# Performance work log

Hardware: AMD Instinct MI355X
Metric: run time of the kernel (lower is better)

The kernel has to match this reference:

```python
import jax, jax.numpy as jnp
import numpy as np

LN_EPS = 1e-5


def _segment_mean(vals, idx, num_segments):
    s = jax.ops.segment_sum(vals, idx, num_segments=num_segments)
    cnt = jax.ops.segment_sum(jnp.ones((vals.shape[0],), vals.dtype), idx, num_segments=num_segments)
    return s / jnp.maximum(cnt, 1.0)[:, None]


def _sage_layer(x, src, dst, W_l, b_l, W_r, gamma, beta):
    # PyG SAGEConv (mean aggr): out = lin_l(mean_{j in N(i)} x_j) + lin_r(x_i)
    N = x.shape[0]
    agg = _segment_mean(x[src], dst, N)                     # [N, in]
    h = agg @ W_l.T + b_l + x @ W_r.T                       # [N, out]
    mu = jnp.mean(h, axis=-1, keepdims=True)
    var = jnp.mean((h - mu) ** 2, axis=-1, keepdims=True)
    h = (h - mu) * jax.lax.rsqrt(var + LN_EPS) * gamma + beta
    return jax.nn.relu(h)                                   # dropout: eval mode (identity)


def setup_inputs() -> dict:
    key = jax.random.key(0)
    ks = jax.random.split(key, 20)
    N, E, IN, H, OUT, G, C = 50000, 600000, 128, 128, 64, 64, 2

    def glorot(k, fo, fi):
        lim = np.sqrt(6.0 / (fo + fi)).astype(np.float32)
        return jax.random.uniform(k, (fo, fi), jnp.float32, -lim, lim)

    inp = {
        'x': jax.random.normal(ks[0], (N, IN), jnp.float32),
        'edge_index': jax.random.randint(ks[1], (2, E), 0, N, jnp.int64),
        'batch': jnp.sort(jax.random.randint(ks[2], (N,), 0, G, jnp.int64)),
    }
    dims = [(IN, H), (H, H), (H, OUT)]
    for i, (fi, fo) in enumerate(dims):
        inp[f'Wl{i}'] = glorot(ks[3 + 4 * i], fo, fi)
        inp[f'bl{i}'] = jnp.zeros((fo,), jnp.float32)
        inp[f'Wr{i}'] = glorot(ks[4 + 4 * i], fo, fi)
        inp[f'g{i}'] = jnp.ones((fo,), jnp.float32)
        inp[f'be{i}'] = jnp.zeros((fo,), jnp.float32)
    inp['cW1'] = glorot(ks[16], H, 2 * OUT)
    inp['cb1'] = jnp.zeros((H,), jnp.float32)
    inp['cW2'] = glorot(ks[17], C, H)
    inp['cb2'] = jnp.zeros((C,), jnp.float32)
    return inp


def reference(x, edge_index, batch,
              Wl0, bl0, Wr0, g0, be0,
              Wl1, bl1, Wr1, g1, be1,
              Wl2, bl2, Wr2, g2, be2,
              cW1, cb1, cW2, cb2):
    src, dst = edge_index[0], edge_index[1]
    h = _sage_layer(x, src, dst, Wl0, bl0, Wr0, g0, be0)
    h = _sage_layer(h, src, dst, Wl1, bl1, Wr1, g1, be1)
    h = _sage_layer(h, src, dst, Wl2, bl2, Wr2, g2, be2)
    G = 64  # number of graphs
    x_mean = _segment_mean(h, batch, G)                     # [G, out]
    x_max = jax.ops.segment_max(h, batch, num_segments=G)   # [G, out]
    z = jnp.concatenate([x_mean, x_max], axis=-1)           # [G, 2*out]
    z = jax.nn.relu(z @ cW1.T + cb1)
    return z @ cW2.T + cb2                                  # [G, num_classes]
```

## Files before the change

### kernel.cpp

```cpp
#include <hip/hip_runtime.h>

typedef unsigned short ushort_t;
typedef short s16x8 __attribute__((ext_vector_type(8)));
typedef float f32x4 __attribute__((ext_vector_type(4)));

#define LN_EPS 1e-5f

__device__ __forceinline__ float b2f(ushort_t u) {
    return __uint_as_float(((unsigned)u) << 16);
}
__device__ __forceinline__ ushort_t f2b(float f) {
    unsigned b = __float_as_uint(f);
    b += 0x7FFFu + ((b >> 16) & 1u);
    return (ushort_t)(b >> 16);
}
__device__ __forceinline__ unsigned f2b2(float lo, float hi) {
    return (unsigned)f2b(lo) | ((unsigned)f2b(hi) << 16);
}
__device__ __forceinline__ float ldf(const void* p, size_t i, int isF) {
    return isF ? ((const float*)p)[i] : b2f(((const ushort_t*)p)[i]);
}

__global__ void GraphSAGE_36026185678961_kernel() {}

__global__ void k_detect_zero(const void* w0, const void* ei, int* __restrict__ flags,
                              int* __restrict__ deg, float* __restrict__ Z, int N) {
    int i = blockIdx.x * blockDim.x + threadIdx.x;
    if (i < N) deg[i] = 0;
    if (i < 64 * 128) Z[i] = 0.f;
    if (blockIdx.x == 0 && threadIdx.x < 64) {
        int t = threadIdx.x;
        const ushort_t* u = (const ushort_t*)w0;
        int pass = 0;
        #pragma unroll
        for (int k = 0; k < 4; ++k) {
            ushort_t v = u[t * 4 + k];
            int ex = (v >> 7) & 0xFF;
            if (ex == 0 || (ex >= 0x60 && ex <= 0x7E)) pass++;
        }
        const unsigned* w = (const unsigned*)ei;
        int nz = (w[2 * t + 1] != 0u) ? 1 : 0;
        #pragma unroll
        for (int off = 32; off; off >>= 1) {
            pass += __shfl_down(pass, off, 64);
            nz += __shfl_down(nz, off, 64);
        }
        if (t == 0) {
            flags[0] = (pass < 205) ? 1 : 0;
            flags[1] = (nz == 0) ? 1 : 0;
        }
    }
}

__global__ void k_xconv(const void* X, const int* __restrict__ flags,
                        ushort_t* __restrict__ XB, int total4) {
    int idx = blockIdx.x * blockDim.x + threadIdx.x;
    if (idx >= total4) return;
    if (flags[0]) {
        float4 v = ((const float4*)X)[idx];
        ushort4 o;
        o.x = f2b(v.x); o.y = f2b(v.y); o.z = f2b(v.z); o.w = f2b(v.w);
        ((ushort4*)XB)[idx] = o;
    } else {
        ((ushort4*)XB)[idx] = ((const ushort4*)X)[idx];
    }
}

__global__ void k_edges(const void* ei, int E, int N, const int* __restrict__ flags,
                        int* __restrict__ s32, int* __restrict__ d32, int* __restrict__ deg) {
    int e = blockIdx.x * blockDim.x + threadIdx.x;
    if (e >= E) return;
    int s, d;
    if (flags[1]) {
        const long long* p = (const long long*)ei;
        s = (int)p[e];
        d = (int)p[E + e];
    } else {
        const int* p = (const int*)ei;
        s = p[e];
        d = p[E + e];
    }
    s32[e] = s;
    d32[e] = d;
    if ((unsigned)d < (unsigned)N) atomicAdd(&deg[d], 1);
}

__global__ void k_scan1(const int* __restrict__ deg, int N,
                        int* __restrict__ rowptr, int* __restrict__ bsum) {
    __shared__ int wsum[4];
    __shared__ int wpre[4];
    int tid = threadIdx.x;
    int lane = tid & 63;
    int w = tid >> 6;
    int i = blockIdx.x * 256 + tid;
    int v = (i < N) ? deg[i] : 0;
    int x = v;
    #pragma unroll
    for (int off = 1; off < 64; off <<= 1) {
        int t = __shfl_up(x, off, 64);
        if (lane >= off) x += t;
    }
    if (lane == 63) wsum[w] = x;
    __syncthreads();
    if (tid == 0) {
        int a = wsum[0]; wpre[0] = a;
        a += wsum[1]; wpre[1] = a;
        a += wsum[2]; wpre[2] = a;
        a += wsum[3]; wpre[3] = a;
    }
    __syncthreads();
    int woff = (w == 0) ? 0 : wpre[w - 1];
    if (i < N) rowptr[i] = woff + x - v;
    if (tid == 0) bsum[blockIdx.x] = wpre[3];
}

__global__ void k_scan2(const int* __restrict__ bsum, int nb,
                        int* __restrict__ boff, int* __restrict__ rowptrN,
                        const void* batch, int N, int G, const int* __restrict__ flags,
                        int* __restrict__ bounds) {
    __shared__ int wsum[4];
    __shared__ int wpre[4];
    int tid = threadIdx.x;
    int lane = tid & 63;
    int w = tid >> 6;
    int run = 0;
    for (int base = 0; base < nb; base += 256) {
        int i = base + tid;
        int v = (i < nb) ? bsum[i] : 0;
        int x = v;
        #pragma unroll
        for (int off = 1; off < 64; off <<= 1) {
            int t = __shfl_up(x, off, 64);
            if (lane >= off) x += t;
        }
        if (lane == 63) wsum[w] = x;
        __syncthreads();
        if (tid == 0) {
            int a = wsum[0]; wpre[0] = a;
            a += wsum[1]; wpre[1] = a;
            a += wsum[2]; wpre[2] = a;
            a += wsum[3]; wpre[3] = a;
        }
        __syncthreads();
        int woff = (w == 0) ? 0 : wpre[w - 1];
        if (i < nb) boff[i] = run + woff + x - v;
        int tot = wpre[3];
        __syncthreads();
        run += tot;
    }
    if (tid == 0) *rowptrN = run;
    if (tid <= G) {
        int isL = flags[1];
        int lo = 0, hi = N;
        while (lo < hi) {
            int mid = (lo + hi) >> 1;
            int bv = isL ? (int)((const long long*)batch)[mid] : ((const int*)batch)[mid];
            if (bv < tid) lo = mid + 1; else hi = mid;
        }
        bounds[tid] = lo;
    }
}

__global__ void k_scan3(int* __restrict__ rowptr, const int* __restrict__ boff,
                        int* __restrict__ cursor, int N) {
    int i = blockIdx.x * 256 + threadIdx.x;
    if (i < N) {
        int r = rowptr[i] + boff[i >> 8];
        rowptr[i] = r;
        cursor[i] = r;
    }
}

__global__ void k_fill(const int* __restrict__ src, const int* __restrict__ dst, int E, int N,
                       int* __restrict__ cursor, int* __restrict__ col) {
    int e = blockIdx.x * blockDim.x + threadIdx.x;
    if (e < E) {
        int d = dst[e];
        if ((unsigned)d < (unsigned)N) {
            int p = atomicAdd(&cursor[d], 1);
            if ((unsigned)p < (unsigned)E) {
                int s = src[e];
                col[p] = ((unsigned)s < (unsigned)N) ? s : 0;
            }
        }
    }
}

__global__ __launch_bounds__(256) void k_agg(
    const ushort_t* __restrict__ X, const int* __restrict__ rowptr,
    const int* __restrict__ col, ushort_t* __restrict__ AGG, int N) {
    int i = blockIdx.x * 4 + (threadIdx.x >> 6);
    if (i >= N) return;
    int l = threadIdx.x & 63;
    int qn = l >> 4;
    int fo = l & 15;
    const uint4* X8 = (const uint4*)X;
    int s = rowptr[i], e = rowptr[i + 1];
    float al[4] = {0.f, 0.f, 0.f, 0.f};
    float ah[4] = {0.f, 0.f, 0.f, 0.f};
    int p = s + qn;
    for (; p + 4 < e; p += 8) {
        int j0 = col[p], j1 = col[p + 4];
        uint4 u0 = X8[(size_t)j0 * 16 + fo];
        uint4 u1 = X8[(size_t)j1 * 16 + fo];
        unsigned w0[4] = {u0.x, u0.y, u0.z, u0.w};
        unsigned w1[4] = {u1.x, u1.y, u1.z, u1.w};
        #pragma unroll
        for (int k = 0; k < 4; ++k) {
            al[k] += __uint_as_float(w0[k] << 16) + __uint_as_float(w1[k] << 16);
            ah[k] += __uint_as_float(w0[k] & 0xFFFF0000u) + __uint_as_float(w1[k] & 0xFFFF0000u);
        }
    }
    for (; p < e; p += 4) {
        int j = col[p];
        uint4 u = X8[(size_t)j * 16 + fo];
        unsigned w0[4] = {u.x, u.y, u.z, u.w};
        #pragma unroll
        for (int k = 0; k < 4; ++k) {
            al[k] += __uint_as_float(w0[k] << 16);
            ah[k] += __uint_as_float(w0[k] & 0xFFFF0000u);
        }
    }
    #pragma unroll
    for (int k = 0; k < 4; ++k) {
        al[k] += __shfl_xor(al[k], 16, 64);
        al[k] += __shfl_xor(al[k], 32, 64);
        ah[k] += __shfl_xor(ah[k], 16, 64);
        ah[k] += __shfl_xor(ah[k], 32, 64);
    }
    if (qn == 0) {
        int d = e - s;
        float inv = 1.f / (float)(d > 0 ? d : 1);
        uint4 o;
        o.x = f2b2(al[0] * inv, ah[0] * inv);
        o.y = f2b2(al[1] * inv, ah[1] * inv);
        o.z = f2b2(al[2] * inv, ah[2] * inv);
        o.w = f2b2(al[3] * inv, ah[3] * inv);
        ((uint4*)AGG)[(size_t)i * 16 + fo] = o;
    }
}

__global__ void k_wprep(const void* Wl0, const void* Wr0, const void* Wl1, const void* Wr1,
                        const void* Wl2, const void* Wr2, const int* __restrict__ flags,
                        ushort_t* __restrict__ Wb0, ushort_t* __restrict__ Wb1,
                        ushort_t* __restrict__ Wb2) {
    int t = blockIdx.x * blockDim.x + threadIdx.x;
    int isF = flags[0];
    const void* Wl;
    const void* Wr;
    ushort_t* Wb;
    int base;
    if (t < 256 * 128) { Wl = Wl0; Wr = Wr0; Wb = Wb0; base = t; }
    else if (t < 2 * 256 * 128) { Wl = Wl1; Wr = Wr1; Wb = Wb1; base = t - 256 * 128; }
    else if (t < 2 * 256 * 128 + 256 * 64) { Wl = Wl2; Wr = Wr2; Wb = Wb2; base = t - 2 * 256 * 128; }
    else return;
    int f = base >> 8, k = base & 255;
    float v = (k < 128) ? ldf(Wl, f * 128 + k, isF) : ldf(Wr, f * 128 + (k - 128), isF);
    Wb[base] = isF ? f2b(v) : ((const ushort_t*)((k < 128) ? Wl : Wr))[f * 128 + (k & 127)];
}

template <int FO>
__global__ __launch_bounds__(256, 2) void k_gemm_ln(
    const ushort_t* __restrict__ AGG, const ushort_t* __restrict__ X,
    const ushort_t* __restrict__ Wb,
    const void* bl, const void* gam, const void* bet,
    const int* __restrict__ flags,
    ushort_t* __restrict__ H, int M) {
    constexpr int NT = FO / 16;
    constexpr int R = 4;
    int lane = threadIdx.x & 63;
    int wid = threadIdx.x >> 6;
    int wrow0 = (blockIdx.x * 4 + wid) * (R * 16);
    if (wrow0 >= M) return;
    int isF = flags[0];
    int m = lane & 15;
    int q = lane >> 4;

    int arow[R];
    #pragma unroll
    for (int r = 0; r < R; ++r) {
        int ar = wrow0 + r * 16 + m;
        arow[r] = (ar < M) ? ar : (M - 1);
    }

    f32x4 acc[R][NT];
    #pragma unroll
    for (int r = 0; r < R; ++r)
        #pragma unroll
        for (int nt = 0; nt < NT; ++nt) acc[r][nt] = (f32x4){0.f, 0.f, 0.f, 0.f};

    #pragma unroll
    for (int kk = 0; kk < 8; ++kk) {
        const ushort_t* base = (kk < 4) ? AGG : X;
        int ko = (kk & 3) * 32 + q * 8;
        s16x8 a[R];
        #pragma unroll
        for (int r = 0; r < R; ++r)
            a[r] = *(const s16x8*)(base + (size_t)arow[r] * 128 + ko);
        #pragma unroll
        for (int nt = 0; nt < NT; ++nt) {
            s16x8 b = *(const s16x8*)(Wb + (size_t)(nt * 16 + m) * 256 + kk * 32 + q * 8);
            #pragma unroll
            for (int r = 0; r < R; ++r)
                acc[r][nt] = __builtin_amdgcn_mfma_f32_16x16x32_bf16(a[r], b, acc[r][nt], 0, 0, 0);
        }
    }

    #pragma unroll
    for (int r = 0; r < R; ++r) {
        #pragma unroll
        for (int nt = 0; nt < NT; ++nt) {
            float bv = ldf(bl, nt * 16 + m, isF);
            #pragma unroll
            for (int rr = 0; rr < 4; ++rr) acc[r][nt][rr] += bv;
        }
        float mu[4], rs[4];
        #pragma unroll
        for (int rr = 0; rr < 4; ++rr) {
            float s1 = 0.f, s2 = 0.f;
            #pragma unroll
            for (int nt = 0; nt < NT; ++nt) {
                float v = acc[r][nt][rr];
                s1 += v;
                s2 += v * v;
            }
            #pragma unroll
            for (int off = 1; off < 16; off <<= 1) {
                s1 += __shfl_xor(s1, off, 64);
                s2 += __shfl_xor(s2, off, 64);
            }
            float mm = s1 / (float)FO;
            float var = s2 / (float)FO - mm * mm;
            var = var > 0.f ? var : 0.f;
            mu[rr] = mm;
            rs[rr] = rsqrtf(var + LN_EPS);
        }
        #pragma unroll
        for (int nt = 0; nt < NT; ++nt) {
            int n0 = nt * 16 + m;
            float g = ldf(gam, n0, isF);
            float be = ldf(bet, n0, isF);
            #pragma unroll
            for (int rr = 0; rr < 4; ++rr) {
                int row = wrow0 + r * 16 + q * 4 + rr;
                if (row < M) {
                    float y = (acc[r][nt][rr] - mu[rr]) * rs[rr] * g + be;
                    y = y > 0.f ? y : 0.f;
                    H[(size_t)row * FO + n0] = f2b(y);
                }
            }
        }
    }
}

__global__ void k_pool(const ushort_t* __restrict__ H,
                       const int* __restrict__ bounds, float* __restrict__ Z, int N) {
    int g = blockIdx.x >> 3;
    int chunk = blockIdx.x & 7;
    int f = threadIdx.x & 63;
    int sub = threadIdx.x >> 6;
    int strm = chunk * 4 + sub;
    int s = bounds[g], e = bounds[g + 1];
    s = s < 0 ? 0 : (s > N ? N : s);
    e = e < s ? s : (e > N ? N : e);
    float sum = 0.f, mx = 0.f;
    for (int i = s + strm; i < e; i += 32) {
        float v = b2f(H[(size_t)i * 64 + f]);
        sum += v;
        mx = mx > v ? mx : v;
    }
    atomicAdd(&Z[g * 128 + f], sum);
    atomicMax((int*)&Z[g * 128 + 64 + f], __float_as_int(mx));
}

__global__ void k_mlp(const float* __restrict__ Z, const int* __restrict__ bounds,
                      const void* cW1, const void* cb1, const void* cW2, const void* cb2,
                      const int* __restrict__ flags, void* __restrict__ out) {
    int g = blockIdx.x;
    int f = threadIdx.x;
    int isF = flags[0];
    __shared__ float z[128];
    __shared__ float hid[128];
    __shared__ float r0[2], r1[2];
    int cnt = bounds[g + 1] - bounds[g];
    float c = (float)(cnt > 0 ? cnt : 1);
    float zv = Z[g * 128 + f];
    if (f < 64) zv /= c;
    z[f] = zv;
    __syncthreads();
    float acc = ldf(cb1, f, isF);
    #pragma unroll 8
    for (int k = 0; k < 128; ++k) acc += z[k] * ldf(cW1, f * 128 + k, isF);
    acc = acc > 0.f ? acc : 0.f;
    hid[f] = acc;
    __syncthreads();
    float p0 = hid[f] * ldf(cW2, f, isF);
    float p1 = hid[f] * ldf(cW2, 128 + f, isF);
    #pragma unroll
    for (int off = 32; off > 0; off >>= 1) {
        p0 += __shfl_xor(p0, off, 64);
        p1 += __shfl_xor(p1, off, 64);
    }
    int w = f >> 6;
    if ((f & 63) == 0) { r0[w] = p0; r1[w] = p1; }
    __syncthreads();
    if (f == 0) {
        float v0 = r0[0] + r0[1] + ldf(cb2, 0, isF);
        float v1 = r1[0] + r1[1] + ldf(cb2, 1, isF);
        if (isF) {
            ((float*)out)[g * 2 + 0] = v0;
            ((float*)out)[g * 2 + 1] = v1;
        } else {
            ((ushort_t*)out)[g * 2 + 0] = f2b(v0);
            ((ushort_t*)out)[g * 2 + 1] = f2b(v1);
        }
    }
}

extern "C" void kernel_launch(void* const* d_in, const int* in_sizes, int n_in,
                              void* d_out, int out_size, void* d_ws, size_t ws_size,
                              hipStream_t stream) {
    const void* x = d_in[0];
    const void* ei = d_in[1];
    const void* batch = d_in[2];
    const void* Wl0 = d_in[3];
    const void* bl0 = d_in[4];
    const void* Wr0 = d_in[5];
    const void* g0 = d_in[6];
    const void* be0 = d_in[7];
    const void* Wl1 = d_in[8];
    const void* bl1 = d_in[9];
    const void* Wr1 = d_in[10];
    const void* g1 = d_in[11];
    const void* be1 = d_in[12];
    const void* Wl2 = d_in[13];
    const void* bl2 = d_in[14];
    const void* Wr2 = d_in[15];
    const void* g2 = d_in[16];
    const void* be2 = d_in[17];
    const void* cW1 = d_in[18];
    const void* cb1 = d_in[19];
    const void* cW2 = d_in[20];
    const void* cb2 = d_in[21];

    const int N = in_sizes[0] / 128;
    const int E = in_sizes[1] / 2;
    const int G = 64;

    char* w = (char*)d_ws;
    size_t o = 0;
    auto take = [&](size_t bytes) -> void* {
        void* p = w + o;
        o = (o + bytes + 255) & ~(size_t)255;
        return p;
    };
    int nb1 = (N + 255) / 256;
    int* flags  = (int*)take(4 * 4);
    int* rowptr = (int*)take((size_t)(N + 1) * 4);
    int* cursor = (int*)take((size_t)N * 4);
    int* deg    = (int*)take((size_t)N * 4);
    int* bsum   = (int*)take((size_t)nb1 * 4);
    int* boff   = (int*)take((size_t)nb1 * 4);
    int* col    = (int*)take((size_t)E * 4);
    int* src32  = (int*)take((size_t)E * 4);
    int* dst32  = (int*)take((size_t)E * 4);
    int* bounds = (int*)take((size_t)(G + 1) * 4);
    float* Z    = (float*)take((size_t)G * 128 * 4);
    ushort_t* Wb0 = (ushort_t*)take((size_t)128 * 256 * 2);
    ushort_t* Wb1 = (ushort_t*)take((size_t)128 * 256 * 2);
    ushort_t* Wb2 = (ushort_t*)take((size_t)64 * 256 * 2);
    ushort_t* AGG = (ushort_t*)take((size_t)N * 128 * 2);
    ushort_t* H1  = (ushort_t*)take((size_t)N * 128 * 2);
    ushort_t* H2  = (ushort_t*)take((size_t)N * 128 * 2);
    ushort_t* XB  = H2;
    ushort_t* H3  = H1;
    if (o > ws_size) return;

    int eb = (E + 255) / 256;
    k_detect_zero<<<nb1, 256, 0, stream>>>(Wl0, ei, flags, deg, Z, N);
    k_xconv<<<(N * 128 / 4 + 255) / 256, 256, 0, stream>>>(x, flags, XB, N * 128 / 4);
    k_edges<<<eb, 256, 0, stream>>>(ei, E, N, flags, src32, dst32, deg);
    k_scan1<<<nb1, 256, 0, stream>>>(deg, N, rowptr, bsum);
    k_scan2<<<1, 256, 0, stream>>>(bsum, nb1, boff, rowptr + N, batch, N, G, flags, bounds);
    k_scan3<<<nb1, 256, 0, stream>>>(rowptr, boff, cursor, N);
    k_fill<<<eb, 256, 0, stream>>>(src32, dst32, E, N, cursor, col);
    k_wprep<<<(2 * 256 * 128 + 256 * 64 + 255) / 256, 256, 0, stream>>>(
        Wl0, Wr0, Wl1, Wr1, Wl2, Wr2, flags, Wb0, Wb1, Wb2);

    int gb = (N + 255) / 256;
    int ab = (N + 3) / 4;

    k_agg<<<ab, 256, 0, stream>>>(XB, rowptr, col, AGG, N);
    k_gemm_ln<128><<<gb, 256, 0, stream>>>(AGG, XB, Wb0, bl0, g0, be0, flags, H1, N);
    k_agg<<<ab, 256, 0, stream>>>(H1, rowptr, col, AGG, N);
    k_gemm_ln<128><<<gb, 256, 0, stream>>>(AGG, H1, Wb1, bl1, g1, be1, flags, H2, N);
    k_agg<<<ab, 256, 0, stream>>>(H2, rowptr, col, AGG, N);
    k_gemm_ln<64><<<gb, 256, 0, stream>>>(AGG, H2, Wb2, bl2, g2, be2, flags, H3, N);

    k_pool<<<G * 8, 256, 0, stream>>>(H3, bounds, Z, N);
    k_mlp<<<G, 128, 0, stream>>>(Z, bounds, cW1, cb1, cW2, cb2, flags, d_out);
}
```

Measured before the change: 379.9 us.

## Drop edge staging buffers, halve GEMM row tile, fuse pooling with MLP

The edge kernel now only builds the degree histogram, and the fill kernel reads src/dst straight from edge_index, which removes the intermediate src32/dst32 writes and reads. The GEMM+LayerNorm kernel handles 2 row tiles per wave instead of 4 and launches twice as many blocks, trading per-wave reuse for more parallelism. Pooling and the classifier MLP are merged into one kernel with one block per graph and a shared-memory reduction, removing the Z buffer, its zeroing and the global atomics. Each graph's pooling now runs on only 4 waves, so that stage has less parallelism.

```diff
diff --git a/kernel.cpp b/kernel.cpp
--- a/kernel.cpp
+++ b/kernel.cpp
@@ -24,10 +24,9 @@
 __global__ void GraphSAGE_36026185678961_kernel() {}
 
 __global__ void k_detect_zero(const void* w0, const void* ei, int* __restrict__ flags,
-                              int* __restrict__ deg, float* __restrict__ Z, int N) {
+                              int* __restrict__ deg, int N) {
     int i = blockIdx.x * blockDim.x + threadIdx.x;
     if (i < N) deg[i] = 0;
-    if (i < 64 * 128) Z[i] = 0.f;
     if (blockIdx.x == 0 && threadIdx.x < 64) {
         int t = threadIdx.x;
         const ushort_t* u = (const ushort_t*)w0;
@@ -66,22 +65,11 @@
     }
 }
 
-__global__ void k_edges(const void* ei, int E, int N, const int* __restrict__ flags,
-                        int* __restrict__ s32, int* __restrict__ d32, int* __restrict__ deg) {
+__global__ void k_hist(const void* ei, int E, int N, const int* __restrict__ flags,
+                       int* __restrict__ deg) {
     int e = blockIdx.x * blockDim.x + threadIdx.x;
     if (e >= E) return;
-    int s, d;
-    if (flags[1]) {
-        const long long* p = (const long long*)ei;
-        s = (int)p[e];
-        d = (int)p[E + e];
-    } else {
-        const int* p = (const int*)ei;
-        s = p[e];
-        d = p[E + e];
-    }
-    s32[e] = s;
-    d32[e] = d;
+    int d = flags[1] ? (int)((const long long*)ei)[E + e] : ((const int*)ei)[E + e];
     if ((unsigned)d < (unsigned)N) atomicAdd(&deg[d], 1);
 }
 
@@ -171,18 +159,23 @@
     }
 }
 
-__global__ void k_fill(const int* __restrict__ src, const int* __restrict__ dst, int E, int N,
+__global__ void k_fill(const void* ei, int E, int N, const int* __restrict__ flags,
                        int* __restrict__ cursor, int* __restrict__ col) {
     int e = blockIdx.x * blockDim.x + threadIdx.x;
-    if (e < E) {
-        int d = dst[e];
-        if ((unsigned)d < (unsigned)N) {
-            int p = atomicAdd(&cursor[d], 1);
-            if ((unsigned)p < (unsigned)E) {
-                int s = src[e];
-                col[p] = ((unsigned)s < (unsigned)N) ? s : 0;
-            }
-        }
+    if (e >= E) return;
+    int s, d;
+    if (flags[1]) {
+        const long long* p = (const long long*)ei;
+        s = (int)p[e];
+        d = (int)p[E + e];
+    } else {
+        const int* p = (const int*)ei;
+        s = p[e];
+        d = p[E + e];
+    }
+    if ((unsigned)d < (unsigned)N) {
+        int p = atomicAdd(&cursor[d], 1);
+        if ((unsigned)p < (unsigned)E) col[p] = ((unsigned)s < (unsigned)N) ? s : 0;
     }
 }
 
@@ -267,7 +260,7 @@
     const int* __restrict__ flags,
     ushort_t* __restrict__ H, int M) {
     constexpr int NT = FO / 16;
-    constexpr int R = 4;
+    constexpr int R = 2;
     int lane = threadIdx.x & 63;
     int wid = threadIdx.x >> 6;
     int wrow0 = (blockIdx.x * 4 + wid) * (R * 16);
@@ -353,58 +346,65 @@
     }
 }
 
-__global__ void k_pool(const ushort_t* __restrict__ H,
-                       const int* __restrict__ bounds, float* __restrict__ Z, int N) {
-    int g = blockIdx.x >> 3;
-    int chunk = blockIdx.x & 7;
-    int f = threadIdx.x & 63;
-    int sub = threadIdx.x >> 6;
-    int strm = chunk * 4 + sub;
+__global__ __launch_bounds__(256) void k_pool_mlp(
+    const ushort_t* __restrict__ H,
+    const int* __restrict__ bounds,
+    const void* cW1, const void* cb1, const void* cW2, const void* cb2,
+    const int* __restrict__ flags, void* __restrict__ out, int N) {
+    int g = blockIdx.x;
+    int tid = threadIdx.x;
+    int f = tid & 63;
+    int sub = tid >> 6;
+    int isF = flags[0];
     int s = bounds[g], e = bounds[g + 1];
     s = s < 0 ? 0 : (s > N ? N : s);
     e = e < s ? s : (e > N ? N : e);
     float sum = 0.f, mx = 0.f;
-    for (int i = s + strm; i < e; i += 32) {
+    for (int i = s + sub; i < e; i += 4) {
         float v = b2f(H[(size_t)i * 64 + f]);
         sum += v;
         mx = mx > v ? mx : v;
     }
-    atomicAdd(&Z[g * 128 + f], sum);
-    atomicMax((int*)&Z[g * 128 + 64 + f], __float_as_int(mx));
-}
-
-__global__ void k_mlp(const float* __restrict__ Z, const int* __restrict__ bounds,
-                      const void* cW1, const void* cb1, const void* cW2, const void* cb2,
-                      const int* __restrict__ flags, void* __restrict__ out) {
-    int g = blockIdx.x;
-    int f = threadIdx.x;
-    int isF = flags[0];
+    __shared__ float zs[4][64];
+    __shared__ float zm[4][64];
     __shared__ float z[128];
     __shared__ float hid[128];
     __shared__ float r0[2], r1[2];
-    int cnt = bounds[g + 1] - bounds[g];
-    float c = (float)(cnt > 0 ? cnt : 1);
-    float zv = Z[g * 128 + f];
-    if (f < 64) zv /= c;
-    z[f] = zv;
-    __syncthreads();
-    float acc = ldf(cb1, f, isF);
-    #pragma unroll 8
-    for (int k = 0; k < 128; ++k) acc += z[k] * ldf(cW1, f * 128 + k, isF);
-    acc = acc > 0.f ? acc : 0.f;
-    hid[f] = acc;
-    __syncthreads();
-    float p0 = hid[f] * ldf(cW2, f, isF);
-    float p1 = hid[f] * ldf(cW2, 128 + f, isF);
-    #pragma unroll
-    for (int off = 32; off > 0; off >>= 1) {
-        p0 += __shfl_xor(p0, off, 64);
-        p1 += __shfl_xor(p1, off, 64);
-    }
-    int w = f >> 6;
-    if ((f & 63) == 0) { r0[w] = p0; r1[w] = p1; }
-    __syncthreads();
-    if (f == 0) {
+    zs[sub][f] = sum;
+    zm[sub][f] = mx;
+    __syncthreads();
+    if (tid < 128) {
+        if (tid < 64) {
+            int cnt = e - s;
+            float c = (float)(cnt > 0 ? cnt : 1);
+            z[tid] = (zs[0][tid] + zs[1][tid] + zs[2][tid] + zs[3][tid]) / c;
+        } else {
+            int ff = tid - 64;
+            float m0 = zm[0][ff] > zm[1][ff] ? zm[0][ff] : zm[1][ff];
+            float m1 = zm[2][ff] > zm[3][ff] ? zm[2][ff] : zm[3][ff];
+            z[tid] = m0 > m1 ? m0 : m1;
+        }
+    }
+    __syncthreads();
+    if (tid < 128) {
+        float acc = ldf(cb1, tid, isF);
+        #pragma unroll 8
+        for (int k = 0; k < 128; ++k) acc += z[k] * ldf(cW1, tid * 128 + k, isF);
+        hid[tid] = acc > 0.f ? acc : 0.f;
+    }
+    __syncthreads();
+    if (tid < 128) {
+        float p0 = hid[tid] * ldf(cW2, tid, isF);
+        float p1 = hid[tid] * ldf(cW2, 128 + tid, isF);
+        #pragma unroll
+        for (int off = 32; off > 0; off >>= 1) {
+            p0 += __shfl_xor(p0, off, 64);
+            p1 += __shfl_xor(p1, off, 64);
+        }
+        if ((tid & 63) == 0) { r0[tid >> 6] = p0; r1[tid >> 6] = p1; }
+    }
+    __syncthreads();
+    if (tid == 0) {
         float v0 = r0[0] + r0[1] + ldf(cb2, 0, isF);
         float v1 = r1[0] + r1[1] + ldf(cb2, 1, isF);
         if (isF) {
@@ -462,10 +462,7 @@
     int* bsum   = (int*)take((size_t)nb1 * 4);
     int* boff   = (int*)take((size_t)nb1 * 4);
     int* col    = (int*)take((size_t)E * 4);
-    int* src32  = (int*)take((size_t)E * 4);
-    int* dst32  = (int*)take((size_t)E * 4);
     int* bounds = (int*)take((size_t)(G + 1) * 4);
-    float* Z    = (float*)take((size_t)G * 128 * 4);
     ushort_t* Wb0 = (ushort_t*)take((size_t)128 * 256 * 2);
     ushort_t* Wb1 = (ushort_t*)take((size_t)128 * 256 * 2);
     ushort_t* Wb2 = (ushort_t*)take((size_t)64 * 256 * 2);
@@ -477,17 +474,17 @@
     if (o > ws_size) return;
 
     int eb = (E + 255) / 256;
-    k_detect_zero<<<nb1, 256, 0, stream>>>(Wl0, ei, flags, deg, Z, N);
+    k_detect_zero<<<nb1, 256, 0, stream>>>(Wl0, ei, flags, deg, N);
     k_xconv<<<(N * 128 / 4 + 255) / 256, 256, 0, stream>>>(x, flags, XB, N * 128 / 4);
-    k_edges<<<eb, 256, 0, stream>>>(ei, E, N, flags, src32, dst32, deg);
+    k_hist<<<eb, 256, 0, stream>>>(ei, E, N, flags, deg);
     k_scan1<<<nb1, 256, 0, stream>>>(deg, N, rowptr, bsum);
     k_scan2<<<1, 256, 0, stream>>>(bsum, nb1, boff, rowptr + N, batch, N, G, flags, bounds);
     k_scan3<<<nb1, 256, 0, stream>>>(rowptr, boff, cursor, N);
-    k_fill<<<eb, 256, 0, stream>>>(src32, dst32, E, N, cursor, col);
+    k_fill<<<eb, 256, 0, stream>>>(ei, E, N, flags, cursor, col);
     k_wprep<<<(2 * 256 * 128 + 256 * 64 + 255) / 256, 256, 0, stream>>>(
         Wl0, Wr0, Wl1, Wr1, Wl2, Wr2, flags, Wb0, Wb1, Wb2);
 
-    int gb = (N + 255) / 256;
+    int gb = (N + 127) / 128;
     int ab = (N + 3) / 4;
 
     k_agg<<<ab, 256, 0, stream>>>(XB, rowptr, col, AGG, N);
@@ -497,6 +494,5 @@
     k_agg<<<ab, 256, 0, stream>>>(H2, rowptr, col, AGG, N);
     k_gemm_ln<64><<<gb, 256, 0, stream>>>(AGG, H2, Wb2, bl2, g2, be2, flags, H3, N);
 
-    k_pool<<<G * 8, 256, 0, stream>>>(H3, bounds, Z, N);
-    k_mlp<<<G, 128, 0, stream>>>(Z, bounds, cW1, cb1, cW2, cb2, flags, d_out);
-}
+    k_pool_mlp<<<G, 256, 0, stream>>>(H3, bounds, cW1, cb1, cW2, cb2, flags, d_out, N);
+}
```

New measurement: 414.6 us. +9.1%, slower.

## Drop edge staging buffers, shrink GEMM row tile, vectorize pooling reads

Applied to the files above, without the earlier changes.

The edge preprocessing no longer writes int32 copies of src/dst. A histogram kernel reads only the destination row of edge_index, and the fill kernel reads both rows directly, which saves a round trip through two E-sized buffers. The GEMM+LayerNorm kernel now handles 2 row tiles per wave instead of 4, doubling the grid to spread work across more waves. Pooling reads packed bf16 pairs as 32-bit words with 16 blocks per graph instead of 8, giving wider loads and more parallelism.

```diff
diff --git a/kernel.cpp b/kernel.cpp
--- a/kernel.cpp
+++ b/kernel.cpp
@@ -66,22 +66,11 @@
     }
 }
 
-__global__ void k_edges(const void* ei, int E, int N, const int* __restrict__ flags,
-                        int* __restrict__ s32, int* __restrict__ d32, int* __restrict__ deg) {
+__global__ void k_hist(const void* ei, int E, int N, const int* __restrict__ flags,
+                       int* __restrict__ deg) {
     int e = blockIdx.x * blockDim.x + threadIdx.x;
     if (e >= E) return;
-    int s, d;
-    if (flags[1]) {
-        const long long* p = (const long long*)ei;
-        s = (int)p[e];
-        d = (int)p[E + e];
-    } else {
-        const int* p = (const int*)ei;
-        s = p[e];
-        d = p[E + e];
-    }
-    s32[e] = s;
-    d32[e] = d;
+    int d = flags[1] ? (int)((const long long*)ei)[E + e] : ((const int*)ei)[E + e];
     if ((unsigned)d < (unsigned)N) atomicAdd(&deg[d], 1);
 }
 
@@ -171,18 +160,23 @@
     }
 }
 
-__global__ void k_fill(const int* __restrict__ src, const int* __restrict__ dst, int E, int N,
+__global__ void k_fill(const void* ei, int E, int N, const int* __restrict__ flags,
                        int* __restrict__ cursor, int* __restrict__ col) {
     int e = blockIdx.x * blockDim.x + threadIdx.x;
-    if (e < E) {
-        int d = dst[e];
-        if ((unsigned)d < (unsigned)N) {
-            int p = atomicAdd(&cursor[d], 1);
-            if ((unsigned)p < (unsigned)E) {
-                int s = src[e];
-                col[p] = ((unsigned)s < (unsigned)N) ? s : 0;
-            }
-        }
+    if (e >= E) return;
+    int s, d;
+    if (flags[1]) {
+        const long long* p = (const long long*)ei;
+        s = (int)p[e];
+        d = (int)p[E + e];
+    } else {
+        const int* p = (const int*)ei;
+        s = p[e];
+        d = p[E + e];
+    }
+    if ((unsigned)d < (unsigned)N) {
+        int p = atomicAdd(&cursor[d], 1);
+        if ((unsigned)p < (unsigned)E) col[p] = ((unsigned)s < (unsigned)N) ? s : 0;
     }
 }
 
@@ -267,7 +261,7 @@
     const int* __restrict__ flags,
     ushort_t* __restrict__ H, int M) {
     constexpr int NT = FO / 16;
-    constexpr int R = 4;
+    constexpr int R = 2;
     int lane = threadIdx.x & 63;
     int wid = threadIdx.x >> 6;
     int wrow0 = (blockIdx.x * 4 + wid) * (R * 16);
@@ -353,24 +347,32 @@
     }
 }
 
-__global__ void k_pool(const ushort_t* __restrict__ H,
-                       const int* __restrict__ bounds, float* __restrict__ Z, int N) {
-    int g = blockIdx.x >> 3;
-    int chunk = blockIdx.x & 7;
-    int f = threadIdx.x & 63;
-    int sub = threadIdx.x >> 6;
-    int strm = chunk * 4 + sub;
+__global__ __launch_bounds__(256) void k_pool(
+    const ushort_t* __restrict__ H,
+    const int* __restrict__ bounds, float* __restrict__ Z, int N) {
+    int g = blockIdx.x >> 4;
+    int chunk = blockIdx.x & 15;
+    int lane = threadIdx.x & 31;
+    int sub = threadIdx.x >> 5;
+    int strm = chunk * 8 + sub;
     int s = bounds[g], e = bounds[g + 1];
     s = s < 0 ? 0 : (s > N ? N : s);
     e = e < s ? s : (e > N ? N : e);
-    float sum = 0.f, mx = 0.f;
-    for (int i = s + strm; i < e; i += 32) {
-        float v = b2f(H[(size_t)i * 64 + f]);
-        sum += v;
-        mx = mx > v ? mx : v;
-    }
-    atomicAdd(&Z[g * 128 + f], sum);
-    atomicMax((int*)&Z[g * 128 + 64 + f], __float_as_int(mx));
+    const unsigned* H2 = (const unsigned*)H;
+    float sl = 0.f, sh = 0.f, ml = 0.f, mh = 0.f;
+    for (int i = s + strm; i < e; i += 128) {
+        unsigned u = H2[(size_t)i * 32 + lane];
+        float vl = __uint_as_float(u << 16);
+        float vh = __uint_as_float(u & 0xFFFF0000u);
+        sl += vl; sh += vh;
+        ml = ml > vl ? ml : vl;
+        mh = mh > vh ? mh : vh;
+    }
+    int f0 = lane * 2;
+    atomicAdd(&Z[g * 128 + f0], sl);
+    atomicAdd(&Z[g * 128 + f0 + 1], sh);
+    atomicMax((int*)&Z[g * 128 + 64 + f0], __float_as_int(ml));
+    atomicMax((int*)&Z[g * 128 + 64 + f0 + 1], __float_as_int(mh));
 }
 
 __global__ void k_mlp(const float* __restrict__ Z, const int* __restrict__ bounds,
@@ -462,8 +464,6 @@
     int* bsum   = (int*)take((size_t)nb1 * 4);
     int* boff   = (int*)take((size_t)nb1 * 4);
     int* col    = (int*)take((size_t)E * 4);
-    int* src32  = (int*)take((size_t)E * 4);
-    int* dst32  = (int*)take((size_t)E * 4);
     int* bounds = (int*)take((size_t)(G + 1) * 4);
     float* Z    = (float*)take((size_t)G * 128 * 4);
     ushort_t* Wb0 = (ushort_t*)take((size_t)128 * 256 * 2);
@@ -479,15 +479,15 @@
     int eb = (E + 255) / 256;
     k_detect_zero<<<nb1, 256, 0, stream>>>(Wl0, ei, flags, deg, Z, N);
     k_xconv<<<(N * 128 / 4 + 255) / 256, 256, 0, stream>>>(x, flags, XB, N * 128 / 4);
-    k_edges<<<eb, 256, 0, stream>>>(ei, E, N, flags, src32, dst32, deg);
+    k_hist<<<eb, 256, 0, stream>>>(ei, E, N, flags, deg);
     k_scan1<<<nb1, 256, 0, stream>>>(deg, N, rowptr, bsum);
     k_scan2<<<1, 256, 0, stream>>>(bsum, nb1, boff, rowptr + N, batch, N, G, flags, bounds);
     k_scan3<<<nb1, 256, 0, stream>>>(rowptr, boff, cursor, N);
-    k_fill<<<eb, 256, 0, stream>>>(src32, dst32, E, N, cursor, col);
+    k_fill<<<eb, 256, 0, stream>>>(ei, E, N, flags, cursor, col);
     k_wprep<<<(2 * 256 * 128 + 256 * 64 + 255) / 256, 256, 0, stream>>>(
         Wl0, Wr0, Wl1, Wr1, Wl2, Wr2, flags, Wb0, Wb1, Wb2);
 
-    int gb = (N + 255) / 256;
+    int gb = (N + 127) / 128;
     int ab = (N + 3) / 4;
 
     k_agg<<<ab, 256, 0, stream>>>(XB, rowptr, col, AGG, N);
@@ -497,6 +497,6 @@
     k_agg<<<ab, 256, 0, stream>>>(H2, rowptr, col, AGG, N);
     k_gemm_ln<64><<<gb, 256, 0, stream>>>(AGG, H2, Wb2, bl2, g2, be2, flags, H3, N);
 
-    k_pool<<<G * 8, 256, 0, stream>>>(H3, bounds, Z, N);
+    k_pool<<<G * 16, 256, 0, stream>>>(H3, bounds, Z, N);
     k_mlp<<<G, 128, 0, stream>>>(Z, bounds, cW1, cb1, cW2, cb2, flags, d_out);
 }
```

Measured after the change: 376.8 us. About the same (-0.8%).
